# Kernel optimization log

Measured on AMD Instinct MI355X. Metric: run time of the kernel, lower is better.

## Reference

```python
import jax, jax.numpy as jnp
import numpy as np

COUNTS = [1536, 8192, 16384, 24576, 12288, 1024, 512, 512, 256, 128, 128]
OFFS = np.concatenate([[0], np.cumsum(COUNTS)]).astype(int).tolist()
N = OFFS[-1]          # 65536 atoms total, sorted by degree
MAX_DEG = 10
BATCH = 2048          # fixed GraphGather batch size
F_IN = 75
GC = 256
DENSE = 512
N_TASKS = 12
N_CLASSES = 2
BN_EPS = 1e-3         # keras BatchNormalization default epsilon


def _graph_conv(x, deg_adjs, w0, wself, wneigh, b):
    # deepchem GraphConv: per-degree (self @ Wself + sum_neighbors @ Wneigh + b), relu
    outs = [x[OFFS[0]:OFFS[1]] @ w0 + b[0]]  # degree-0 atoms: self transform only
    for d in range(1, MAX_DEG + 1):
        self_atoms = x[OFFS[d]:OFFS[d + 1]]            # [n_d, F]
        neigh = x[deg_adjs[d - 1]].sum(axis=1)         # gather [n_d, d, F] -> sum -> [n_d, F]
        outs.append(self_atoms @ wself[d - 1] + neigh @ wneigh[d - 1] + b[d])
    return jax.nn.relu(jnp.concatenate(outs, axis=0))


def _graph_pool(x, deg_adjs):
    # deepchem GraphPool: elementwise max over {self} U neighbors, per degree
    outs = [x[OFFS[0]:OFFS[1]]]  # degree-0 atoms pass through
    for d in range(1, MAX_DEG + 1):
        self_atoms = x[OFFS[d]:OFFS[d + 1]]
        outs.append(jnp.maximum(self_atoms, x[deg_adjs[d - 1]].max(axis=1)))
    return jnp.concatenate(outs, axis=0)


def _bn(x, g, bta, m, v):
    # inference-mode BatchNormalization (training=False -> moving stats)
    return g * (x - m) * jax.lax.rsqrt(v + BN_EPS) + bta


def setup_inputs():
    key = jax.random.key(0)
    ks = iter(jax.random.split(key, 64))
    inp = {}
    inp["atom_features"] = jax.random.normal(next(ks), (N, F_IN), jnp.float32)
    inp["degree_slice"] = jnp.asarray(
        np.stack([np.array(OFFS[:-1]), np.array(COUNTS)], axis=1), jnp.int32)
    # each molecule gets exactly N/BATCH atoms so no GraphGather segment is empty
    inp["membership"] = jax.random.permutation(
        next(ks), jnp.arange(N, dtype=jnp.int32) % BATCH)
    inp["n_samples"] = BATCH
    for d in range(1, MAX_DEG + 1):
        inp["deg_adj_%d" % d] = jax.random.randint(
            next(ks), (COUNTS[d], d), 0, N, jnp.int32)

    def lin(k, fi, fo):
        return jax.random.normal(k, (fi, fo), jnp.float32) * np.float32(1.0 / np.sqrt(fi))

    for li, fi in [(1, F_IN), (2, GC)]:
        inp["gc%d_w0" % li] = lin(next(ks), fi, GC)
        inp["gc%d_wself" % li] = jnp.stack([lin(next(ks), fi, GC) for _ in range(MAX_DEG)])
        inp["gc%d_wneigh" % li] = jnp.stack([lin(next(ks), fi, GC) for _ in range(MAX_DEG)])
        inp["gc%d_b" % li] = jnp.zeros((MAX_DEG + 1, GC), jnp.float32)
    for bi, dim in [(1, GC), (2, GC), (3, DENSE)]:
        inp["bn%d_gamma" % bi] = jnp.ones((dim,), jnp.float32)
        inp["bn%d_beta" % bi] = jnp.zeros((dim,), jnp.float32)
        inp["bn%d_mean" % bi] = jnp.zeros((dim,), jnp.float32)
        inp["bn%d_var" % bi] = jnp.ones((dim,), jnp.float32)
    inp["dense_w"] = lin(next(ks), GC, DENSE)
    inp["dense_b"] = jnp.zeros((DENSE,), jnp.float32)
    inp["out_w"] = lin(next(ks), 2 * DENSE, N_TASKS * N_CLASSES)
    inp["out_b"] = jnp.zeros((N_TASKS * N_CLASSES,), jnp.float32)
    return inp


def reference(atom_features, degree_slice, membership, n_samples,
              deg_adj_1, deg_adj_2, deg_adj_3, deg_adj_4, deg_adj_5,
              deg_adj_6, deg_adj_7, deg_adj_8, deg_adj_9, deg_adj_10,
              gc1_w0, gc1_wself, gc1_wneigh, gc1_b,
              gc2_w0, gc2_wself, gc2_wneigh, gc2_b,
              bn1_gamma, bn1_beta, bn1_mean, bn1_var,
              bn2_gamma, bn2_beta, bn2_mean, bn2_var,
              bn3_gamma, bn3_beta, bn3_mean, bn3_var,
              dense_w, dense_b, out_w, out_b):
    deg_adjs = [deg_adj_1, deg_adj_2, deg_adj_3, deg_adj_4, deg_adj_5,
                deg_adj_6, deg_adj_7, deg_adj_8, deg_adj_9, deg_adj_10]
    h = _graph_conv(atom_features, deg_adjs, gc1_w0, gc1_wself, gc1_wneigh, gc1_b)
    h = _bn(h, bn1_gamma, bn1_beta, bn1_mean, bn1_var)
    h = _graph_pool(h, deg_adjs)
    h = _graph_conv(h, deg_adjs, gc2_w0, gc2_wself, gc2_wneigh, gc2_b)
    h = _bn(h, bn2_gamma, bn2_beta, bn2_mean, bn2_var)
    h = _graph_pool(h, deg_adjs)
    h = jax.nn.relu(h @ dense_w + dense_b)
    h = _bn(h, bn3_gamma, bn3_beta, bn3_mean, bn3_var)
    # GraphGather: tanh(concat(segment_sum, segment_max))
    ssum = jax.ops.segment_sum(h, membership, num_segments=BATCH)
    smax = jax.ops.segment_max(h, membership, num_segments=BATCH)
    fp = jnp.tanh(jnp.concatenate([ssum, smax], axis=1))   # [BATCH, 2*DENSE]
    logits = (fp @ out_w + out_b).reshape(BATCH, N_TASKS, N_CLASSES)[:n_samples]
    probs = jax.nn.softmax(logits, axis=-1)
    return probs, logits, fp
```

## Files before the change

### kernel.cpp

```cpp
#include <hip/hip_runtime.h>
#include <hip/hip_fp16.h>
#include <math.h>

#define NATOMS 65536

typedef _Float16 f16_t;
typedef __attribute__((ext_vector_type(8))) _Float16 half8;
typedef __attribute__((ext_vector_type(4))) float f32x4;

__constant__ int c_offs[12] = {0,1536,9728,26112,50688,62976,64000,64512,65024,65280,65408,65536};

struct Adj { const int* p[10]; };

__device__ __forceinline__ int seg_of(int row) {
    int s = 0;
#pragma unroll
    for (int i = 1; i <= 10; ++i) s += (row >= c_offs[i]) ? 1 : 0;
    return s;
}

__device__ __forceinline__ void glds16(const f16_t* g, f16_t* l) {
    __builtin_amdgcn_global_load_lds(
        (const __attribute__((address_space(1))) unsigned int*)g,
        (__attribute__((address_space(3))) unsigned int*)l,
        16, 0, 0);
}


__global__ void pack_w1(const float* __restrict__ w0, const float* __restrict__ wself,
                        const float* __restrict__ wneigh, f16_t* __restrict__ Wp) {
    int idx = blockIdx.x * 256 + threadIdx.x;
    int j = idx & 7, lane = (idx >> 3) & 63;
    int kb = (idx >> 9) % 6;
    int rest = idx / (512 * 6);
    int ni = rest & 15, s = rest >> 4;
    int k = kb * 32 + (lane >> 4) * 8 + j;
    int n = ni * 16 + (lane & 15);
    float v = 0.f;
    if (k < 75) v = (s == 0) ? w0[k*256 + n] : wself[((s-1)*75 + k)*256 + n];
    else if (k >= 96 && k < 171 && s > 0) v = wneigh[((s-1)*75 + (k-96))*256 + n];
    Wp[idx] = (f16_t)v;
}

__global__ void pack_w2(const float* __restrict__ w0, const float* __restrict__ wself,
                        const float* __restrict__ wneigh, f16_t* __restrict__ Wp) {
    int idx = blockIdx.x * 256 + threadIdx.x;
    int j = idx & 7, lane = (idx >> 3) & 63;
    int kb = (idx >> 9) & 15;
    int rest = idx >> 13;
    int ni = rest & 15, s = rest >> 4;
    int k = kb * 32 + (lane >> 4) * 8 + j;
    int n = ni * 16 + (lane & 15);
    float v = 0.f;
    if (k < 256) v = (s == 0) ? w0[k*256 + n] : wself[((s-1)*256 + k)*256 + n];
    else if (s > 0) v = wneigh[((s-1)*256 + (k-256))*256 + n];
    Wp[idx] = (f16_t)v;
}

__global__ void pack_wd(const float* __restrict__ w, f16_t* __restrict__ Wp) {
    int idx = blockIdx.x * 256 + threadIdx.x;
    int j = idx & 7, lane = (idx >> 3) & 63;
    int kb = (idx >> 9) & 7;
    int ni = (idx >> 12) & 31;
    int k = kb * 32 + (lane >> 4) * 8 + j;
    int n = ni * 16 + (lane & 15);
    Wp[idx] = (f16_t)w[(size_t)k*512 + n];
}

__global__ void pack_wo(const float* __restrict__ w, f16_t* __restrict__ Wp) {
    int idx = blockIdx.x * 256 + threadIdx.x;
    int j = idx & 7, lane = (idx >> 3) & 63;
    int kb = (idx >> 9) & 31;
    int ni = idx >> 14;
    int k = kb * 32 + (lane >> 4) * 8 + j;
    int n = ni * 16 + (lane & 15);
    Wp[idx] = (n < 24) ? (f16_t)w[k*24 + n] : (f16_t)0.f;
}

__global__ void cvt_pad(const float* __restrict__ xf,
                        f16_t* __restrict__ xq_rm, f16_t* __restrict__ xq_bl) {
    int idx = blockIdx.x * 256 + threadIdx.x;
    int r = idx / 12;
    int cc = idx - r * 12;
    int c = cc << 3;
    f16_t o[8];
#pragma unroll
    for (int e = 0; e < 8; ++e)
        o[e] = (c + e < 75) ? (f16_t)xf[(size_t)r*75 + c + e] : (f16_t)0.f;
    *(uint4*)(xq_rm + (size_t)r*96 + c) = *(uint4*)o;
    *(uint4*)(xq_bl + (size_t)(r>>4)*1536 + (c>>5)*512 + ((c>>3)&3)*128 + (r&15)*8) = *(uint4*)o;
}

template<int D, bool ISMAX, int LD>
__device__ __forceinline__ void gathD(float* v, const f16_t* __restrict__ src,
                                      const int* __restrict__ ap, int c) {
    int rows[D];
#pragma unroll
    for (int j = 0; j < D; ++j) rows[j] = ap[j];
    uint4 raw[D];
#pragma unroll
    for (int j = 0; j < D; ++j) raw[j] = *(const uint4*)(src + (size_t)rows[j]*LD + c);
#pragma unroll
    for (int j = 0; j < D; ++j) {
        const f16_t* u = (const f16_t*)&raw[j];
#pragma unroll
        for (int e = 0; e < 8; ++e) {
            float f = (float)u[e];
            v[e] = ISMAX ? fmaxf(v[e], f) : (v[e] + f);
        }
    }
}

template<bool ISMAX, int LD>
__device__ __forceinline__ void gath_switch(float* v, const f16_t* __restrict__ src,
                                            const int* __restrict__ ap, int s, int c) {
    switch (s) {
        case 1:  gathD<1,ISMAX,LD>(v,src,ap,c);  break;
        case 2:  gathD<2,ISMAX,LD>(v,src,ap,c);  break;
        case 3:  gathD<3,ISMAX,LD>(v,src,ap,c);  break;
        case 4:  gathD<4,ISMAX,LD>(v,src,ap,c);  break;
        case 5:  gathD<5,ISMAX,LD>(v,src,ap,c);  break;
        case 6:  gathD<6,ISMAX,LD>(v,src,ap,c);  break;
        case 7:  gathD<7,ISMAX,LD>(v,src,ap,c);  break;
        case 8:  gathD<8,ISMAX,LD>(v,src,ap,c);  break;
        case 9:  gathD<9,ISMAX,LD>(v,src,ap,c);  break;
        case 10: gathD<10,ISMAX,LD>(v,src,ap,c); break;
        default: break;
    }
}

__global__ __launch_bounds__(256) void nbsum_x(const f16_t* __restrict__ xq_rm,
                                               f16_t* __restrict__ NBX, Adj adj) {
    int idx = blockIdx.x * 256 + threadIdx.x;
    int r = idx >> 4;
    int cc = idx & 15;
    if (cc >= 12) return;
    int c = cc << 3;
    int s = seg_of(r);
    float v[8];
#pragma unroll
    for (int e = 0; e < 8; ++e) v[e] = 0.f;
    if (s > 0)
        gath_switch<false,96>(v, xq_rm, adj.p[s-1] + (size_t)(r - c_offs[s]) * s, s, c);
    f16_t o[8];
#pragma unroll
    for (int e = 0; e < 8; ++e) o[e] = (f16_t)v[e];
    *(uint4*)(NBX + (size_t)(r>>4)*1536 + (c>>5)*512 + ((c>>3)&3)*128 + (r&15)*8) = *(uint4*)o;
}

template<bool DUAL>
__global__ __launch_bounds__(256) void pool_k(const f16_t* __restrict__ H,
                                              f16_t* __restrict__ P_bl,
                                              f16_t* __restrict__ P_rm, Adj adj) {
    int idx = blockIdx.x * 256 + threadIdx.x;
    int r = idx >> 5;
    int c = (idx & 31) << 3;
    int s = seg_of(r);
    uint4 self = *(const uint4*)(H + (size_t)r*256 + c);
    const f16_t* hp = (const f16_t*)&self;
    float v[8];
#pragma unroll
    for (int e = 0; e < 8; ++e) v[e] = (float)hp[e];
    if (s > 0)
        gath_switch<true,256>(v, H, adj.p[s-1] + (size_t)(r - c_offs[s]) * s, s, c);
    f16_t o[8];
#pragma unroll
    for (int e = 0; e < 8; ++e) o[e] = (f16_t)v[e];
    *(uint4*)(P_bl + (size_t)(r>>4)*4096 + (c>>5)*512 + ((c>>3)&3)*128 + (r&15)*8) = *(uint4*)o;
    if (DUAL)
        *(uint4*)(P_rm + (size_t)r*256 + c) = *(uint4*)o;
}

__global__ __launch_bounds__(256) void nbsum_k(const f16_t* __restrict__ P_rm,
                                               f16_t* __restrict__ NB, Adj adj) {
    int idx = blockIdx.x * 256 + threadIdx.x;
    int r = idx >> 5;
    int c = (idx & 31) << 3;
    int s = seg_of(r);
    float v[8];
#pragma unroll
    for (int e = 0; e < 8; ++e) v[e] = 0.f;
    if (s > 0)
        gath_switch<false,256>(v, P_rm, adj.p[s-1] + (size_t)(r - c_offs[s]) * s, s, c);
    f16_t o[8];
#pragma unroll
    for (int e = 0; e < 8; ++e) o[e] = (f16_t)v[e];
    *(uint4*)(NB + (size_t)(r>>4)*4096 + (c>>5)*512 + ((c>>3)&3)*128 + (r&15)*8) = *(uint4*)o;
}

template<int NKB, int KSPB, int NKBA0, int NKBA1, int N, int NY, bool SEG>
__global__ __launch_bounds__(256)
void gemm_mfma(const f16_t* __restrict__ A0, const f16_t* __restrict__ A1,
               const f16_t* __restrict__ Wp,
               const float* __restrict__ bias,
               const float* __restrict__ bng, const float* __restrict__ bnb,
               const float* __restrict__ bnm, const float* __restrict__ bnv,
               f16_t* __restrict__ C)
{
    constexpr int NNT = N / 16;
    __shared__ char smem[32768];
    f16_t* sm = (f16_t*)smem;
    f16_t* eps = (f16_t*)smem;

    const int t = threadIdx.x;
    const int lane = t & 63, wave = t >> 6;
    const int wm = wave >> 1, wn = wave & 1;
    const int quad = lane >> 4, l16 = lane & 15;
    const int id = blockIdx.x;
    const int xcd = id & 7;
    const int jj = id >> 3;
    const int xi = jj / NY;
    const int y  = jj - xi * NY;
    const int r0 = (xi * 8 + xcd) * 128;
    const int n0 = y * 128;
    const int seg = SEG ? seg_of(r0) : 0;
    const int nbase = n0 >> 4;
    const int rtg = r0 >> 4;

    f32x4 acc[4][4];
#pragma unroll
    for (int mi = 0; mi < 4; ++mi)
#pragma unroll
        for (int ni = 0; ni < 4; ++ni) acc[mi][ni] = (f32x4){0.f,0.f,0.f,0.f};

#pragma unroll
    for (int kbp = 0; kbp < NKB/2; ++kbp) {
#pragma unroll
        for (int u = 0; u < 2; ++u) {
            const int kb = kbp*2 + u;
#pragma unroll
            for (int i = 0; i < 2; ++i) {
                const int rt = wave*2 + i;
                const f16_t* asrc = (kb < KSPB)
                    ? A0 + ((size_t)(rtg + rt)*NKBA0 + kb)*512
                    : A1 + ((size_t)(rtg + rt)*NKBA1 + (kb - KSPB))*512;
                glds16(asrc + lane*8, sm + u*4096 + rt*512);
                glds16(Wp + ((size_t)(seg*NNT + nbase + rt)*NKB + kb)*512 + lane*8,
                       sm + 8192 + u*4096 + rt*512);
            }
        }
        __syncthreads();
#pragma unroll
        for (int u = 0; u < 2; ++u) {
            half8 a[4], b[4];
#pragma unroll
            for (int mi = 0; mi < 4; ++mi)
                a[mi] = *(const half8*)(sm + u*4096 + (wm*4 + mi)*512 + lane*8);
#pragma unroll
            for (int ni = 0; ni < 4; ++ni)
                b[ni] = *(const half8*)(sm + 8192 + u*4096 + (wn*4 + ni)*512 + lane*8);
#pragma unroll
            for (int mi = 0; mi < 4; ++mi)
#pragma unroll
                for (int ni = 0; ni < 4; ++ni)
                    acc[mi][ni] = __builtin_amdgcn_mfma_f32_16x16x32_f16(a[mi], b[ni], acc[mi][ni], 0, 0, 0);
        }
        __syncthreads();
    }

#pragma unroll
    for (int p = 0; p < 2; ++p) {
        if (wm == p) {
#pragma unroll
            for (int ni = 0; ni < 4; ++ni) {
                const int lcol = (wn*4 + ni)*16 + l16;
                const int col = n0 + lcol;
                const float scale = bng[col] * rsqrtf(bnv[col] + 1e-3f);
                const float shift = bnb[col] - bnm[col] * scale;
                const float bv = bias[(SEG ? seg*N : 0) + col];
#pragma unroll
                for (int mi = 0; mi < 4; ++mi) {
                    const int lrowb = mi*16 + quad*4;
#pragma unroll
                    for (int r = 0; r < 4; ++r) {
                        float v = acc[mi][ni][r] + bv;
                        v = fmaxf(v, 0.f);
                        v = fmaf(v, scale, shift);
                        eps[(lrowb + r)*136 + lcol] = (f16_t)v;
                    }
                }
            }
        }
        __syncthreads();
#pragma unroll
        for (int it = 0; it < 4; ++it) {
            int row = it*16 + (t >> 4);
            int ch  = t & 15;
            uint4 v = *(const uint4*)&eps[row*136 + ch*8];
            *(uint4*)(C + (size_t)(r0 + p*64 + row)*N + n0 + ch*8) = v;
        }
        __syncthreads();
    }
}

__global__ void scatter_k(const int* __restrict__ mem, int* __restrict__ counts, int* __restrict__ slots) {
    int i = blockIdx.x * 256 + threadIdx.x;
    int s = mem[i];
    int p = atomicAdd(&counts[s], 1);
    if (p < 32) slots[s*32 + p] = i;
}

__global__ __launch_bounds__(64)
void reduce_k(const f16_t* __restrict__ H3, const int* __restrict__ slots,
              float* __restrict__ fp, f16_t* __restrict__ fph) {
    int s = blockIdx.x, l = threadIdx.x;
    int c = l * 8;
    const int* sl = slots + s*32;
    float sm[8], mx[8];
#pragma unroll
    for (int e = 0; e < 8; ++e) { sm[e] = 0.f; mx[e] = -INFINITY; }
#pragma unroll
    for (int i = 0; i < 32; ++i) {
        int a = sl[i];
        uint4 raw = *(const uint4*)(H3 + (size_t)a*512 + c);
        const f16_t* u = (const f16_t*)&raw;
#pragma unroll
        for (int e = 0; e < 8; ++e) {
            float f = (float)u[e];
            sm[e] += f;
            mx[e] = fmaxf(mx[e], f);
        }
    }
    float o1[8], o2[8];
    f16_t h1[8], h2[8];
#pragma unroll
    for (int e = 0; e < 8; ++e) {
        o1[e] = tanhf(sm[e]); o2[e] = tanhf(mx[e]);
        h1[e] = (f16_t)o1[e]; h2[e] = (f16_t)o2[e];
    }
    float* fr = fp + (size_t)s*1024;
    *(float4*)(fr + c)       = *(float4*)&o1[0];
    *(float4*)(fr + c + 4)   = *(float4*)&o1[4];
    *(float4*)(fr + 512 + c)     = *(float4*)&o2[0];
    *(float4*)(fr + 512 + c + 4) = *(float4*)&o2[4];
    f16_t* fh = fph + (size_t)s*1024;
    *(uint4*)(fh + c)       = *(uint4*)h1;
    *(uint4*)(fh + 512 + c) = *(uint4*)h2;
}

__global__ __launch_bounds__(256)
void final_mfma(const f16_t* __restrict__ fph, const f16_t* __restrict__ Wop,
                const float* __restrict__ out_b,
                float* __restrict__ probs, float* __restrict__ logits) {
    const int t = threadIdx.x;
    const int lane = t & 63, wave = t >> 6;
    const int quad = lane >> 4, l16 = lane & 15;
    const int r0 = blockIdx.x * 256 + wave * 64;

    f32x4 acc[4][2];
#pragma unroll
    for (int mi = 0; mi < 4; ++mi)
#pragma unroll
        for (int ni = 0; ni < 2; ++ni) acc[mi][ni] = (f32x4){0.f,0.f,0.f,0.f};

    size_t rowoff[4];
#pragma unroll
    for (int mi = 0; mi < 4; ++mi)
        rowoff[mi] = (size_t)(r0 + mi*16 + l16) * 1024 + quad*8;
    size_t boff[2];
#pragma unroll
    for (int ni = 0; ni < 2; ++ni)
        boff[ni] = (size_t)ni * 32 * 512 + lane*8;

    auto loadA = [&](half8* a, int kb) {
#pragma unroll
        for (int mi = 0; mi < 4; ++mi) a[mi] = *(const half8*)(fph + rowoff[mi] + kb*32);
    };
    auto loadB = [&](half8* b, int kb) {
#pragma unroll
        for (int ni = 0; ni < 2; ++ni) b[ni] = *(const half8*)(Wop + boff[ni] + (size_t)kb*512);
    };
    auto domfma = [&](half8* a, half8* b) {
#pragma unroll
        for (int mi = 0; mi < 4; ++mi)
#pragma unroll
            for (int ni = 0; ni < 2; ++ni)
                acc[mi][ni] = __builtin_amdgcn_mfma_f32_16x16x32_f16(a[mi], b[ni], acc[mi][ni], 0, 0, 0);
    };

    half8 a0[4], b0[2], a1[4], b1[2];
    loadA(a0, 0); loadB(b0, 0);
#pragma unroll
    for (int kb = 0; kb < 32; kb += 2) {
        loadA(a1, kb + 1); loadB(b1, kb + 1);
        domfma(a0, b0);
        if (kb + 2 < 32) { loadA(a0, kb + 2); loadB(b0, kb + 2); }
        domfma(a1, b1);
    }

#pragma unroll
    for (int ni = 0; ni < 2; ++ni) {
        const int c = ni*16 + l16;
        const bool ok = (c < 24);
        const float bv = ok ? out_b[c] : 0.f;
#pragma unroll
        for (int mi = 0; mi < 4; ++mi) {
#pragma unroll
            for (int r = 0; r < 4; ++r) {
                float lg = acc[mi][ni][r] + bv;
                float lp = __shfl_xor(lg, 1);
                float m = fmaxf(lg, lp);
                float e  = expf(lg - m);
                float ep = expf(lp - m);
                float pr = e / (e + ep);
                if (ok) {
                    int row = r0 + mi*16 + quad*4 + r;
                    logits[(size_t)row*24 + c] = lg;
                    probs[(size_t)row*24 + c]  = pr;
                }
            }
        }
    }
}

extern "C" void kernel_launch(void* const* d_in, const int* in_sizes, int n_in,
                              void* d_out, int out_size, void* d_ws, size_t ws_size,
                              hipStream_t stream) {
    const float* atom       = (const float*)d_in[0];
    const int*   membership = (const int*)  d_in[2];
    Adj adj;
    for (int d = 0; d < 10; ++d) adj.p[d] = (const int*)d_in[4+d];
    const float* gc1_w0     = (const float*)d_in[14];
    const float* gc1_wself  = (const float*)d_in[15];
    const float* gc1_wneigh = (const float*)d_in[16];
    const float* gc1_b      = (const float*)d_in[17];
    const float* gc2_w0     = (const float*)d_in[18];
    const float* gc2_wself  = (const float*)d_in[19];
    const float* gc2_wneigh = (const float*)d_in[20];
    const float* gc2_b      = (const float*)d_in[21];
    const float* bn1g = (const float*)d_in[22]; const float* bn1b = (const float*)d_in[23];
    const float* bn1m = (const float*)d_in[24]; const float* bn1v = (const float*)d_in[25];
    const float* bn2g = (const float*)d_in[26]; const float* bn2b = (const float*)d_in[27];
    const float* bn2m = (const float*)d_in[28]; const float* bn2v = (const float*)d_in[29];
    const float* bn3g = (const float*)d_in[30]; const float* bn3b = (const float*)d_in[31];
    const float* bn3m = (const float*)d_in[32]; const float* bn3v = (const float*)d_in[33];
    const float* dense_w = (const float*)d_in[34];
    const float* dense_b = (const float*)d_in[35];
    const float* out_w   = (const float*)d_in[36];
    const float* out_b   = (const float*)d_in[37];

    f16_t* wsb = (f16_t*)d_ws;
    f16_t* xq_rm = wsb;
    f16_t* xq_bl = wsb + 6291456;
    f16_t* NBX   = wsb + 12582912;
    f16_t* H1b   = wsb + 18874368;
    f16_t* P1rm  = wsb + 35651584;
    f16_t* P1bl  = wsb + 52428800;
    f16_t* NB2b  = wsb + 69206016;
    f16_t* H2b   = H1b;
    f16_t* P2bl  = NB2b;
    f16_t* H3b   = wsb + 35651584;
    f16_t* W1p   = wsb + 85983232;
    f16_t* W2p   = wsb + 86523904;
    f16_t* Wdp   = wsb + 87965696;
    f16_t* Wop   = wsb + 88096768;
    f16_t* fph   = wsb + 88129536;
    int*  counts = (int*)(wsb + 90226688);
    int*  slots  = counts + 2048;

    float* outp   = (float*)d_out;
    float* probs  = outp;
    float* logits = outp + 49152;
    float* fp     = outp + 98304;

    pack_w1<<<2112, 256, 0, stream>>>(gc1_w0, gc1_wself, gc1_wneigh, W1p);
    pack_w2<<<5632, 256, 0, stream>>>(gc2_w0, gc2_wself, gc2_wneigh, W2p);
    pack_wd<<<512,  256, 0, stream>>>(dense_w, Wdp);
    pack_wo<<<128,  256, 0, stream>>>(out_w, Wop);

    cvt_pad<<<(NATOMS*12)/256, 256, 0, stream>>>(atom, xq_rm, xq_bl);
    nbsum_x<<<(NATOMS*16)/256, 256, 0, stream>>>(xq_rm, NBX, adj);
    gemm_mfma<6,3,3,3,256,2,true><<<1024, 256, 0, stream>>>(
        xq_bl, NBX, W1p, gc1_b, bn1g, bn1b, bn1m, bn1v, H1b);
    pool_k<true><<<(NATOMS*32)/256, 256, 0, stream>>>(H1b, P1bl, P1rm, adj);

    nbsum_k<<<(NATOMS*32)/256, 256, 0, stream>>>(P1rm, NB2b, adj);
    gemm_mfma<16,8,8,8,256,2,true><<<1024, 256, 0, stream>>>(
        P1bl, NB2b, W2p, gc2_b, bn2g, bn2b, bn2m, bn2v, H2b);
    pool_k<false><<<(NATOMS*32)/256, 256, 0, stream>>>(H2b, P2bl, nullptr, adj);

    gemm_mfma<8,8,8,8,512,4,false><<<2048, 256, 0, stream>>>(
        P2bl, P2bl, Wdp, dense_b, bn3g, bn3b, bn3m, bn3v, H3b);

    hipMemsetAsync((void*)counts, 0, 2048*sizeof(int), stream);
    scatter_k<<<NATOMS/256, 256, 0, stream>>>(membership, counts, slots);
    reduce_k<<<2048, 64, 0, stream>>>(H3b, slots, fp, fph);

    final_mfma<<<8, 256, 0, stream>>>(fph, Wop, out_b, probs, logits);
}
```

Before: 387.1 us.

## Merge weight-pack kernels, drop memset and fp16 copy, load GEMM operands directly

Fuses the four weight-packing kernels into one launch that also zeroes the scatter counts, replacing the memset. The GEMM drops its LDS staging via global_load_lds and instead loads A/B fragments straight from global memory into registers with a two-stage software prefetch, removing the per-k-block barriers. The final MFMA now converts the fp32 fingerprint to fp16 on the fly, so reduce_k no longer writes a separate fp16 copy. Without LDS sharing, each wave reloads operands from global memory, which adds redundant traffic across the waves of a block.

```diff
diff --git a/kernel.cpp b/kernel.cpp
--- a/kernel.cpp
+++ b/kernel.cpp
@@ -19,62 +19,57 @@
     return s;
 }
 
-__device__ __forceinline__ void glds16(const f16_t* g, f16_t* l) {
-    __builtin_amdgcn_global_load_lds(
-        (const __attribute__((address_space(1))) unsigned int*)g,
-        (__attribute__((address_space(3))) unsigned int*)l,
-        16, 0, 0);
-}
-
-
-__global__ void pack_w1(const float* __restrict__ w0, const float* __restrict__ wself,
-                        const float* __restrict__ wneigh, f16_t* __restrict__ Wp) {
+
+__global__ void pack_all(const float* __restrict__ g1w0, const float* __restrict__ g1ws,
+                         const float* __restrict__ g1wn,
+                         const float* __restrict__ g2w0, const float* __restrict__ g2ws,
+                         const float* __restrict__ g2wn,
+                         const float* __restrict__ dw, const float* __restrict__ ow,
+                         f16_t* __restrict__ W1p, f16_t* __restrict__ W2p,
+                         f16_t* __restrict__ Wdp, f16_t* __restrict__ Wop,
+                         int* __restrict__ counts) {
     int idx = blockIdx.x * 256 + threadIdx.x;
-    int j = idx & 7, lane = (idx >> 3) & 63;
-    int kb = (idx >> 9) % 6;
-    int rest = idx / (512 * 6);
-    int ni = rest & 15, s = rest >> 4;
-    int k = kb * 32 + (lane >> 4) * 8 + j;
-    int n = ni * 16 + (lane & 15);
-    float v = 0.f;
-    if (k < 75) v = (s == 0) ? w0[k*256 + n] : wself[((s-1)*75 + k)*256 + n];
-    else if (k >= 96 && k < 171 && s > 0) v = wneigh[((s-1)*75 + (k-96))*256 + n];
-    Wp[idx] = (f16_t)v;
-}
-
-__global__ void pack_w2(const float* __restrict__ w0, const float* __restrict__ wself,
-                        const float* __restrict__ wneigh, f16_t* __restrict__ Wp) {
-    int idx = blockIdx.x * 256 + threadIdx.x;
-    int j = idx & 7, lane = (idx >> 3) & 63;
-    int kb = (idx >> 9) & 15;
-    int rest = idx >> 13;
-    int ni = rest & 15, s = rest >> 4;
-    int k = kb * 32 + (lane >> 4) * 8 + j;
-    int n = ni * 16 + (lane & 15);
-    float v = 0.f;
-    if (k < 256) v = (s == 0) ? w0[k*256 + n] : wself[((s-1)*256 + k)*256 + n];
-    else if (s > 0) v = wneigh[((s-1)*256 + (k-256))*256 + n];
-    Wp[idx] = (f16_t)v;
-}
-
-__global__ void pack_wd(const float* __restrict__ w, f16_t* __restrict__ Wp) {
-    int idx = blockIdx.x * 256 + threadIdx.x;
-    int j = idx & 7, lane = (idx >> 3) & 63;
-    int kb = (idx >> 9) & 7;
-    int ni = (idx >> 12) & 31;
-    int k = kb * 32 + (lane >> 4) * 8 + j;
-    int n = ni * 16 + (lane & 15);
-    Wp[idx] = (f16_t)w[(size_t)k*512 + n];
-}
-
-__global__ void pack_wo(const float* __restrict__ w, f16_t* __restrict__ Wp) {
-    int idx = blockIdx.x * 256 + threadIdx.x;
-    int j = idx & 7, lane = (idx >> 3) & 63;
-    int kb = (idx >> 9) & 31;
-    int ni = idx >> 14;
-    int k = kb * 32 + (lane >> 4) * 8 + j;
-    int n = ni * 16 + (lane & 15);
-    Wp[idx] = (n < 24) ? (f16_t)w[k*24 + n] : (f16_t)0.f;
+    if (idx < 2048) counts[idx] = 0;
+    if (idx < 540672) {
+        int j = idx & 7, lane = (idx >> 3) & 63;
+        int kb = (idx >> 9) % 6;
+        int rest = idx / (512 * 6);
+        int ni = rest & 15, s = rest >> 4;
+        int k = kb * 32 + (lane >> 4) * 8 + j;
+        int n = ni * 16 + (lane & 15);
+        float v = 0.f;
+        if (k < 75) v = (s == 0) ? g1w0[k*256 + n] : g1ws[((s-1)*75 + k)*256 + n];
+        else if (k >= 96 && k < 171 && s > 0) v = g1wn[((s-1)*75 + (k-96))*256 + n];
+        W1p[idx] = (f16_t)v;
+    } else if (idx < 1982464) {
+        int i2 = idx - 540672;
+        int j = i2 & 7, lane = (i2 >> 3) & 63;
+        int kb = (i2 >> 9) & 15;
+        int rest = i2 >> 13;
+        int ni = rest & 15, s = rest >> 4;
+        int k = kb * 32 + (lane >> 4) * 8 + j;
+        int n = ni * 16 + (lane & 15);
+        float v = 0.f;
+        if (k < 256) v = (s == 0) ? g2w0[k*256 + n] : g2ws[((s-1)*256 + k)*256 + n];
+        else if (s > 0) v = g2wn[((s-1)*256 + (k-256))*256 + n];
+        W2p[i2] = (f16_t)v;
+    } else if (idx < 2113536) {
+        int i2 = idx - 1982464;
+        int j = i2 & 7, lane = (i2 >> 3) & 63;
+        int kb = (i2 >> 9) & 7;
+        int ni = (i2 >> 12) & 31;
+        int k = kb * 32 + (lane >> 4) * 8 + j;
+        int n = ni * 16 + (lane & 15);
+        Wdp[i2] = (f16_t)dw[(size_t)k*512 + n];
+    } else {
+        int i2 = idx - 2113536;
+        int j = i2 & 7, lane = (i2 >> 3) & 63;
+        int kb = (i2 >> 9) & 31;
+        int ni = i2 >> 14;
+        int k = kb * 32 + (lane >> 4) * 8 + j;
+        int n = ni * 16 + (lane & 15);
+        Wop[i2] = (n < 24) ? (f16_t)ow[k*24 + n] : (f16_t)0.f;
+    }
 }
 
 __global__ void cvt_pad(const float* __restrict__ xf,
@@ -198,9 +193,7 @@
                f16_t* __restrict__ C)
 {
     constexpr int NNT = N / 16;
-    __shared__ char smem[32768];
-    f16_t* sm = (f16_t*)smem;
-    f16_t* eps = (f16_t*)smem;
+    __shared__ f16_t eps[64 * 136];
 
     const int t = threadIdx.x;
     const int lane = t & 63, wave = t >> 6;
@@ -223,43 +216,42 @@
 #pragma unroll
         for (int ni = 0; ni < 4; ++ni) acc[mi][ni] = (f32x4){0.f,0.f,0.f,0.f};
 
-#pragma unroll
-    for (int kbp = 0; kbp < NKB/2; ++kbp) {
-#pragma unroll
-        for (int u = 0; u < 2; ++u) {
-            const int kb = kbp*2 + u;
-#pragma unroll
-            for (int i = 0; i < 2; ++i) {
-                const int rt = wave*2 + i;
-                const f16_t* asrc = (kb < KSPB)
-                    ? A0 + ((size_t)(rtg + rt)*NKBA0 + kb)*512
-                    : A1 + ((size_t)(rtg + rt)*NKBA1 + (kb - KSPB))*512;
-                glds16(asrc + lane*8, sm + u*4096 + rt*512);
-                glds16(Wp + ((size_t)(seg*NNT + nbase + rt)*NKB + kb)*512 + lane*8,
-                       sm + 8192 + u*4096 + rt*512);
-            }
-        }
-        __syncthreads();
-#pragma unroll
-        for (int u = 0; u < 2; ++u) {
-            half8 a[4], b[4];
-#pragma unroll
-            for (int mi = 0; mi < 4; ++mi)
-                a[mi] = *(const half8*)(sm + u*4096 + (wm*4 + mi)*512 + lane*8);
+    auto loadA = [&](half8* a, int kb) {
+        const f16_t* base;
+        size_t rstride;
+        int kbl;
+        if (kb < KSPB) { base = A0; rstride = NKBA0; kbl = kb; }
+        else           { base = A1; rstride = NKBA1; kbl = kb - KSPB; }
+#pragma unroll
+        for (int mi = 0; mi < 4; ++mi)
+            a[mi] = *(const half8*)(base + ((size_t)(rtg + wm*4 + mi)*rstride + kbl)*512 + lane*8);
+    };
+    auto loadB = [&](half8* b, int kb) {
+#pragma unroll
+        for (int ni = 0; ni < 4; ++ni)
+            b[ni] = *(const half8*)(Wp + ((size_t)(seg*NNT + nbase + wn*4 + ni)*NKB + kb)*512 + lane*8);
+    };
+    auto domfma = [&](half8* a, half8* b) {
+#pragma unroll
+        for (int mi = 0; mi < 4; ++mi)
 #pragma unroll
             for (int ni = 0; ni < 4; ++ni)
-                b[ni] = *(const half8*)(sm + 8192 + u*4096 + (wn*4 + ni)*512 + lane*8);
-#pragma unroll
-            for (int mi = 0; mi < 4; ++mi)
-#pragma unroll
-                for (int ni = 0; ni < 4; ++ni)
-                    acc[mi][ni] = __builtin_amdgcn_mfma_f32_16x16x32_f16(a[mi], b[ni], acc[mi][ni], 0, 0, 0);
-        }
-        __syncthreads();
+                acc[mi][ni] = __builtin_amdgcn_mfma_f32_16x16x32_f16(a[mi], b[ni], acc[mi][ni], 0, 0, 0);
+    };
+
+    half8 a0[4], b0[4], a1[4], b1[4];
+    loadA(a0, 0); loadB(b0, 0);
+#pragma unroll
+    for (int kb = 0; kb < NKB; kb += 2) {
+        loadA(a1, kb + 1); loadB(b1, kb + 1);
+        domfma(a0, b0);
+        if (kb + 2 < NKB) { loadA(a0, kb + 2); loadB(b0, kb + 2); }
+        domfma(a1, b1);
     }
 
 #pragma unroll
     for (int p = 0; p < 2; ++p) {
+        if (p) __syncthreads();
         if (wm == p) {
 #pragma unroll
             for (int ni = 0; ni < 4; ++ni) {
@@ -289,7 +281,6 @@
             uint4 v = *(const uint4*)&eps[row*136 + ch*8];
             *(uint4*)(C + (size_t)(r0 + p*64 + row)*N + n0 + ch*8) = v;
         }
-        __syncthreads();
     }
 }
 
@@ -302,7 +293,7 @@
 
 __global__ __launch_bounds__(64)
 void reduce_k(const f16_t* __restrict__ H3, const int* __restrict__ slots,
-              float* __restrict__ fp, f16_t* __restrict__ fph) {
+              float* __restrict__ fp) {
     int s = blockIdx.x, l = threadIdx.x;
     int c = l * 8;
     const int* sl = slots + s*32;
@@ -322,24 +313,19 @@
         }
     }
     float o1[8], o2[8];
-    f16_t h1[8], h2[8];
 #pragma unroll
     for (int e = 0; e < 8; ++e) {
         o1[e] = tanhf(sm[e]); o2[e] = tanhf(mx[e]);
-        h1[e] = (f16_t)o1[e]; h2[e] = (f16_t)o2[e];
     }
     float* fr = fp + (size_t)s*1024;
     *(float4*)(fr + c)       = *(float4*)&o1[0];
     *(float4*)(fr + c + 4)   = *(float4*)&o1[4];
     *(float4*)(fr + 512 + c)     = *(float4*)&o2[0];
     *(float4*)(fr + 512 + c + 4) = *(float4*)&o2[4];
-    f16_t* fh = fph + (size_t)s*1024;
-    *(uint4*)(fh + c)       = *(uint4*)h1;
-    *(uint4*)(fh + 512 + c) = *(uint4*)h2;
 }
 
 __global__ __launch_bounds__(256)
-void final_mfma(const f16_t* __restrict__ fph, const f16_t* __restrict__ Wop,
+void final_mfma(const float* __restrict__ fp, const f16_t* __restrict__ Wop,
                 const float* __restrict__ out_b,
                 float* __restrict__ probs, float* __restrict__ logits) {
     const int t = threadIdx.x;
@@ -364,7 +350,15 @@
 
     auto loadA = [&](half8* a, int kb) {
 #pragma unroll
-        for (int mi = 0; mi < 4; ++mi) a[mi] = *(const half8*)(fph + rowoff[mi] + kb*32);
+        for (int mi = 0; mi < 4; ++mi) {
+            const float* src = fp + rowoff[mi] + kb*32;
+            float4 u0 = *(const float4*)(src);
+            float4 u1 = *(const float4*)(src + 4);
+            half8 h;
+            h[0] = (f16_t)u0.x; h[1] = (f16_t)u0.y; h[2] = (f16_t)u0.z; h[3] = (f16_t)u0.w;
+            h[4] = (f16_t)u1.x; h[5] = (f16_t)u1.y; h[6] = (f16_t)u1.z; h[7] = (f16_t)u1.w;
+            a[mi] = h;
+        }
     };
     auto loadB = [&](half8* b, int kb) {
 #pragma unroll
@@ -454,8 +448,7 @@
     f16_t* W2p   = wsb + 86523904;
     f16_t* Wdp   = wsb + 87965696;
     f16_t* Wop   = wsb + 88096768;
-    f16_t* fph   = wsb + 88129536;
-    int*  counts = (int*)(wsb + 90226688);
+    int*  counts = (int*)(wsb + 88129536);
     int*  slots  = counts + 2048;
 
     float* outp   = (float*)d_out;
@@ -463,10 +456,10 @@
     float* logits = outp + 49152;
     float* fp     = outp + 98304;
 
-    pack_w1<<<2112, 256, 0, stream>>>(gc1_w0, gc1_wself, gc1_wneigh, W1p);
-    pack_w2<<<5632, 256, 0, stream>>>(gc2_w0, gc2_wself, gc2_wneigh, W2p);
-    pack_wd<<<512,  256, 0, stream>>>(dense_w, Wdp);
-    pack_wo<<<128,  256, 0, stream>>>(out_w, Wop);
+    pack_all<<<8384, 256, 0, stream>>>(gc1_w0, gc1_wself, gc1_wneigh,
+                                       gc2_w0, gc2_wself, gc2_wneigh,
+                                       dense_w, out_w,
+                                       W1p, W2p, Wdp, Wop, counts);
 
     cvt_pad<<<(NATOMS*12)/256, 256, 0, stream>>>(atom, xq_rm, xq_bl);
     nbsum_x<<<(NATOMS*16)/256, 256, 0, stream>>>(xq_rm, NBX, adj);
@@ -482,9 +475,8 @@
     gemm_mfma<8,8,8,8,512,4,false><<<2048, 256, 0, stream>>>(
         P2bl, P2bl, Wdp, dense_b, bn3g, bn3b, bn3m, bn3v, H3b);
 
-    hipMemsetAsync((void*)counts, 0, 2048*sizeof(int), stream);
     scatter_k<<<NATOMS/256, 256, 0, stream>>>(membership, counts, slots);
-    reduce_k<<<2048, 64, 0, stream>>>(H3b, slots, fp, fph);
-
-    final_mfma<<<8, 256, 0, stream>>>(fph, Wop, out_b, probs, logits);
-}
+    reduce_k<<<2048, 64, 0, stream>>>(H3b, slots, fp);
+
+    final_mfma<<<8, 256, 0, stream>>>(fp, Wop, out_b, probs, logits);
+}
```

Measured after the change: 392.5 us. No clear change (+1.4%).
